# Kernel tuning notes

Hardware: AMD Instinct MI355X
Metric: run time of the kernel (lower is better)

Reference implementation:

```python
import jax, jax.numpy as jnp
import numpy as np

RD = 3  # rec_depth


def _conv_block(x, w, b):
    # x: [B, T, C] -> Conv1d(same padding for odd kernel) + ReLU.
    # AdaptiveMaxPool1d(T) on a length-T input is the identity, so it is omitted.
    pad = (w.shape[-1] - 1) // 2
    xc = jnp.transpose(x, (0, 2, 1))  # [B, C, T]
    out = jax.lax.conv_general_dilated(xc, w, (1,), [(pad, pad)],
                                       dimension_numbers=('NCH', 'OIH', 'NCH'))
    out = jax.nn.relu(out + b[None, :, None])
    return jnp.transpose(out, (0, 2, 1))  # [B, T, n_filters]


def _rhn_cell(x_in, s, WH, WT, RHw, RHb, RTw, RTb):
    # Coupled-gate RHN cell: RD micro-steps of gated highway updates.
    preds = []
    for l in range(RD):
        if l == 0:
            h = jnp.tanh(x_in @ WH + s @ RHw[l] + RHb[l])
            t = jax.nn.sigmoid(x_in @ WT + s @ RTw[l] + RTb[l])
        else:
            h = jnp.tanh(s @ RHw[l] + RHb[l])
            t = jax.nn.sigmoid(s @ RTw[l] + RTb[l])
        s = h * t + (1.0 - t) * s
        preds.append(s)
    return s, preds


def _forward(x, y, conv0_w, conv0_b, conv1_w, conv1_b, c2e_w, c2e_b,
             enc_WH, enc_WT, enc_RHw, enc_RHb, enc_RTw, enc_RTb,
             dec_WH, dec_WT, dec_RHw, dec_RHb, dec_RTw, dec_RTb,
             Tk_w, Uk_w, Uk_b, vk_w, vk_b,
             Wt_w, Vt_w, Vt_b, W_w, W_b, V_w, V_b):
    x = _conv_block(x, conv0_w, conv0_b)
    x = _conv_block(x, conv1_w, conv1_b)
    x = x @ c2e_w + c2e_b                          # [B, T, enc_input_size]
    B, T, _ = x.shape
    NE = enc_WH.shape[1]
    ND = dec_WH.shape[1]

    # ---- RHN encoder: scan over time, emit state after every rec-depth step ----
    def enc_step(s, x_t):
        s, preds = _rhn_cell(x_t, s, enc_WH, enc_WT, enc_RHw, enc_RHb, enc_RTw, enc_RTb)
        return s, jnp.stack(preds, axis=-1)        # [B, NE, RD]

    _, hw = jax.lax.scan(enc_step, jnp.zeros((B, NE), x.dtype), jnp.transpose(x, (1, 0, 2)))
    h = jnp.transpose(hw, (1, 0, 2, 3))            # [B, T, NE, RD] == h_T_L

    # Encoder-side attention projections are decoder-time-invariant: precompute.
    Uh = jnp.einsum('btnr,rnm->rbtm', h, Uk_w) + Uk_b[:, None, None, :]  # [RD, B, T, NE]

    # ---- attentive RHN decoder ----
    def dec_step(carry, y_t):
        s, _ = carry
        Ts = jnp.einsum('bd,rdm->rbm', s, Tk_w)    # T_k(s) broadcast over T
        e = jnp.einsum('rbtm,rm->rbt', jnp.tanh(Uh + Ts[:, :, None, :]), vk_w) \
            + vk_b[:, None, None]                  # [RD, B, T]
        alpha = jax.nn.softmax(e, axis=-1)         # softmax over T
        d = jnp.einsum('rbt,btnr->rbn', alpha, h)  # [RD, B, NE]
        d = jnp.transpose(d, (1, 0, 2)).reshape(B, -1)  # [B, RD*NE], k-major blocks
        y_til = y_t @ Wt_w + d @ Vt_w + Vt_b
        s, _ = _rhn_cell(y_til, s, dec_WH, dec_WT, dec_RHw, dec_RHb, dec_RTw, dec_RTb)
        return (s, d), None

    init = (jnp.zeros((B, ND), x.dtype), jnp.zeros((B, RD * NE), x.dtype))
    (s, d), _ = jax.lax.scan(dec_step, init, jnp.transpose(y, (1, 0, 2)))
    return s @ W_w + W_b + d @ V_w + V_b           # [B, target_feats]


def setup_inputs() -> dict:
    ks = jax.random.split(jax.random.key(0), 24)
    B, T, F, TF = 256, 256, 16, 1
    NF, EI, NE, ND, FS = 64, 64, 128, 128, 5

    def rn(i, shape, s=0.1):
        return jax.random.normal(ks[i], shape, jnp.float32) * s

    z = lambda *shape: jnp.zeros(shape, jnp.float32)
    return {
        'x': jax.random.normal(ks[0], (B, T, F), jnp.float32),
        'y': jax.random.normal(ks[1], (B, T, TF), jnp.float32),
        'conv0_w': rn(2, (NF, F, FS)), 'conv0_b': z(NF),
        'conv1_w': rn(3, (NF, NF, FS)), 'conv1_b': z(NF),
        'c2e_w': rn(4, (NF, EI)), 'c2e_b': z(EI),
        'enc_WH': rn(5, (EI, NE)), 'enc_WT': rn(6, (EI, NE)),
        'enc_RHw': rn(7, (RD, NE, NE)), 'enc_RHb': z(RD, NE),
        'enc_RTw': rn(8, (RD, NE, NE)), 'enc_RTb': z(RD, NE),
        'dec_WH': rn(9, (TF, ND)), 'dec_WT': rn(10, (TF, ND)),
        'dec_RHw': rn(11, (RD, ND, ND)), 'dec_RHb': z(RD, ND),
        'dec_RTw': rn(12, (RD, ND, ND)), 'dec_RTb': z(RD, ND),
        'Tk_w': rn(13, (RD, ND, NE)),
        'Uk_w': rn(14, (RD, NE, NE)), 'Uk_b': z(RD, NE),
        'vk_w': rn(15, (RD, NE)), 'vk_b': z(RD),
        'Wt_w': rn(16, (TF, TF)),
        'Vt_w': rn(17, (RD * NE, TF)), 'Vt_b': z(TF),
        'W_w': rn(18, (ND, TF)), 'W_b': z(TF),
        'V_w': rn(19, (RD * NE, TF)), 'V_b': z(TF),
    }


def reference(x, y, conv0_w, conv0_b, conv1_w, conv1_b, c2e_w, c2e_b,
              enc_WH, enc_WT, enc_RHw, enc_RHb, enc_RTw, enc_RTb,
              dec_WH, dec_WT, dec_RHw, dec_RHb, dec_RTw, dec_RTb,
              Tk_w, Uk_w, Uk_b, vk_w, vk_b,
              Wt_w, Vt_w, Vt_b, W_w, W_b, V_w, V_b):
    return _forward(x, y, conv0_w, conv0_b, conv1_w, conv1_b, c2e_w, c2e_b,
                    enc_WH, enc_WT, enc_RHw, enc_RHb, enc_RTw, enc_RTb,
                    dec_WH, dec_WT, dec_RHw, dec_RHb, dec_RTw, dec_RTb,
                    Tk_w, Uk_w, Uk_b, vk_w, vk_b,
                    Wt_w, Vt_w, Vt_b, W_w, W_b, V_w, V_b)
```

## Files before the change

kernel.cpp:

```cpp
#include <hip/hip_runtime.h>
#include <cstdint>

#define DEV __device__ __forceinline__

typedef unsigned short ushort8 __attribute__((ext_vector_type(8)));
typedef unsigned int uint32;

#if __has_builtin(__builtin_amdgcn_rcpf)
DEV float rcp_fast(float x) { return __builtin_amdgcn_rcpf(x); }
#else
DEV float rcp_fast(float x) { return 1.f / x; }
#endif
#if __has_builtin(__builtin_amdgcn_exp2f)
DEV float exp2_fast(float x) { return __builtin_amdgcn_exp2f(x); }
#else
DEV float exp2_fast(float x) { return exp2f(x); }
#endif

DEV float tanh_fast(float x) {
  float z = exp2_fast(x * 2.8853900817779268f);
  return 1.f - 2.f * rcp_fast(z + 1.f);
}
DEV float sigmoid_fast(float x) {
  return rcp_fast(1.f + exp2_fast(-1.4426950408889634f * x));
}

DEV unsigned short f2bf(float f) {
  uint32 u = __float_as_uint(f);
  u += 0x7FFFu + ((u >> 16) & 1u);
  return (unsigned short)(u >> 16);
}
DEV float bf2f(unsigned short s) { return __uint_as_float(((uint32)s) << 16); }
DEV float bf2f_lo(uint32 u) { return __uint_as_float(u << 16); }
DEV float bf2f_hi(uint32 u) { return __uint_as_float(u & 0xFFFF0000u); }

__global__ __launch_bounds__(256) void k_prep(const float* __restrict__ RHw,
                                              const float* __restrict__ RTw,
                                              uint32* __restrict__ out) {
  int i = blockIdx.x * 256 + threadIdx.x;
  if (i >= 49152) return;
  int g = i / 24576, rem = i % 24576;
  int l = rem / 8192, n2 = (rem >> 7) & 63, m = rem & 127;
  const float* W = g ? RTw : RHw;
  float w0 = W[(size_t)(l * 128 + 2 * n2) * 128 + m];
  float w1 = W[(size_t)(l * 128 + 2 * n2 + 1) * 128 + m];
  out[i] = (uint32)f2bf(w0) | ((uint32)f2bf(w1) << 16);
}

__global__ __launch_bounds__(256) void k_conv0(
    const float* __restrict__ x, const float* __restrict__ w,
    const float* __restrict__ bias, float* __restrict__ out) {
  __shared__ float wl[16 * 5 * 64];
  __shared__ float xl[68 * 16];
  const int blk = blockIdx.x;
  const int b = blk >> 2, tt = blk & 3;
  const int tid = threadIdx.x;
  for (int i = tid; i < 5120; i += 256) {
    int o = i / 80, rem = i % 80, ii = rem / 5, kk = rem % 5;
    wl[(ii * 5 + kk) * 64 + o] = w[i];
  }
  const int t0 = tt * 64;
  for (int i = tid; i < 68 * 16; i += 256) {
    int row = i >> 4, c = i & 15;
    int t = t0 - 2 + row;
    xl[i] = (t >= 0 && t < 256) ? x[((b << 8) + t) * 16 + c] : 0.f;
  }
  __syncthreads();
  const int o = tid & 63, tr = tid >> 6;
  for (int j = 0; j < 16; ++j) {
    int tl = tr * 16 + j;
    float acc = bias[o];
#pragma unroll
    for (int kk = 0; kk < 5; ++kk)
#pragma unroll
      for (int ii = 0; ii < 16; ++ii)
        acc += xl[(tl + kk) * 16 + ii] * wl[(ii * 5 + kk) * 64 + o];
    out[((b << 8) + t0 + tl) * 64 + o] = fmaxf(acc, 0.f);
  }
}

__global__ __launch_bounds__(256) void k_conv1(
    const float* __restrict__ in0, const float* __restrict__ w,
    const float* __restrict__ bias, float* __restrict__ out) {
  __shared__ float wl[64 * 5 * 64];
  __shared__ float xl[68 * 64];
  const int blk = blockIdx.x;
  const int b = blk >> 2, tt = blk & 3;
  const int tid = threadIdx.x;
  for (int i = tid; i < 64 * 5 * 64; i += 256) {
    int o = i / 320, rem = i % 320, ii = rem / 5, kk = rem % 5;
    wl[(ii * 5 + kk) * 64 + o] = w[i];
  }
  const int t0 = tt * 64;
  for (int i = tid; i < 68 * 64; i += 256) {
    int row = i >> 6, c = i & 63;
    int t = t0 - 2 + row;
    xl[i] = (t >= 0 && t < 256) ? in0[((b << 8) + t) * 64 + c] : 0.f;
  }
  __syncthreads();
  const int o = tid & 63, tr = tid >> 6;
  for (int j = 0; j < 16; ++j) {
    int tl = tr * 16 + j;
    float acc = bias[o];
    for (int kk = 0; kk < 5; ++kk) {
#pragma unroll 16
      for (int ii = 0; ii < 64; ++ii)
        acc += xl[(tl + kk) * 64 + ii] * wl[(ii * 5 + kk) * 64 + o];
    }
    out[((b << 8) + t0 + tl) * 64 + o] = fmaxf(acc, 0.f);
  }
}

__global__ __launch_bounds__(256) void k_c2e_proj(
    const float* __restrict__ in1, const float* __restrict__ cw,
    const float* __restrict__ cb, const float* __restrict__ WH,
    const float* __restrict__ WT, float* __restrict__ xph,
    float* __restrict__ xpt) {
  __shared__ float xin[64 * 64];
  __shared__ float w1[64 * 64];
  __shared__ float xe[64 * 64];
  __shared__ float wh[64 * 128];
  __shared__ float wt[64 * 128];
  const int blk = blockIdx.x;
  const int b = blk >> 2, tt = blk & 3;
  const int tid = threadIdx.x;
  for (int i = tid; i < 4096; i += 256) {
    xin[i] = in1[(size_t)(((b << 8) + tt * 64)) * 64 + i];
    w1[i] = cw[i];
  }
  for (int i = tid; i < 8192; i += 256) {
    wh[i] = WH[i];
    wt[i] = WT[i];
  }
  __syncthreads();
  {
    const int o = tid & 63, tr = tid >> 6;
    for (int j = 0; j < 16; ++j) {
      int tl = tr * 16 + j;
      float acc = cb[o];
#pragma unroll 16
      for (int k = 0; k < 64; ++k) acc += xin[tl * 64 + k] * w1[k * 64 + o];
      xe[tl * 64 + o] = acc;
    }
  }
  __syncthreads();
  {
    const int m = tid & 127, hf = tid >> 7;
    for (int j = 0; j < 32; ++j) {
      int tl = hf * 32 + j;
      float a0 = 0.f, a1 = 0.f;
#pragma unroll 16
      for (int k = 0; k < 64; ++k) {
        float xv = xe[tl * 64 + k];
        a0 += xv * wh[k * 128 + m];
        a1 += xv * wt[k * 128 + m];
      }
      size_t oidx = (size_t)((b << 8) + tt * 64 + tl) * 128 + m;
      xph[oidx] = a0;
      xpt[oidx] = a1;
    }
  }
}

__global__ __launch_bounds__(512, 2) void k_encoder(
    const float* __restrict__ xph, const float* __restrict__ xpt,
    const float* __restrict__ RHw, const float* __restrict__ RHb,
    const float* __restrict__ RTw, const float* __restrict__ RTb,
    unsigned short* __restrict__ h_bf) {
  const int b = blockIdx.x;
  const int tid = threadIdx.x;
  const int g = tid >> 8;
  const int m = (tid >> 1) & 127;
  const int hf = tid & 1;
  const float* W = g ? RTw : RHw;
  const float* Bb = g ? RTb : RHb;
  const float* XP = g ? xpt : xph;
  float wreg[3][64];
#pragma unroll
  for (int l = 0; l < 3; ++l)
#pragma unroll
    for (int j = 0; j < 64; ++j)
      wreg[l][j] = W[(size_t)(l * 128 + hf * 64 + j) * 128 + m];
  float bias[3];
#pragma unroll
  for (int l = 0; l < 3; ++l) bias[l] = Bb[l * 128 + m];

  __shared__ float s_lds[128];
  __shared__ float hg[128];
  __shared__ float tg[128];
  if (tid < 128) s_lds[tid] = 0.f;
  __syncthreads();

  for (int t = 0; t < 256; ++t) {
    const float xp = XP[(size_t)((b << 8) + t) * 128 + m];
#pragma unroll
    for (int l = 0; l < 3; ++l) {
      float acc = (hf == 0) ? (bias[l] + (l == 0 ? xp : 0.f)) : 0.f;
      const float* sp = s_lds + hf * 64;
#pragma unroll
      for (int j = 0; j < 64; ++j) acc += sp[j] * wreg[l][j];
      float tot = acc + __shfl_xor(acc, 1);
      if (hf == 0) {
        if (g == 0) hg[m] = tanh_fast(tot);
        else        tg[m] = sigmoid_fast(tot);
      }
      __syncthreads();
      if (tid < 128) {
        float tv = tg[tid];
        float sn = hg[tid] * tv + (1.f - tv) * s_lds[tid];
        s_lds[tid] = sn;
        h_bf[((size_t)(b * 3 + t) * 0 + ((size_t)(b * 3 + l) * 256 + t)) * 128 + tid] = f2bf(sn);
      }
      __syncthreads();
    }
  }
}

__global__ __launch_bounds__(256) void k_uh(
    const unsigned short* __restrict__ h_bf, const float* __restrict__ Uk_w,
    const float* __restrict__ Uk_b, unsigned short* __restrict__ Uh_bf) {
  __shared__ float wl[128 * 128];
  __shared__ float hl[32 * 128];
  const int blk = blockIdx.x;
  const int b = blk / 24;
  const int rem = blk % 24;
  const int r = rem >> 3, tt = rem & 7;
  const int tid = threadIdx.x;
  for (int i = tid; i < 16384; i += 256) wl[i] = Uk_w[(size_t)r * 16384 + i];
  const size_t hbase = ((size_t)(b * 3 + r) * 256 + tt * 32) * 128;
  const ushort8* hv = (const ushort8*)(h_bf + hbase);
  for (int i = tid; i < 512; i += 256) {
    ushort8 u = hv[i];
#pragma unroll
    for (int j = 0; j < 8; ++j) hl[i * 8 + j] = bf2f(u[j]);
  }
  __syncthreads();
  const int m = tid & 127, tr = tid >> 7;
  const float ub = Uk_b[r * 128 + m];
  for (int j = 0; j < 16; ++j) {
    int tl = tr * 16 + j;
    float acc = ub;
#pragma unroll 16
    for (int n = 0; n < 128; ++n) acc += hl[tl * 128 + n] * wl[n * 128 + m];
    Uh_bf[hbase + (size_t)tl * 128 + m] = f2bf(acc);
  }
}

__global__ __launch_bounds__(768) void k_hv(
    const unsigned short* __restrict__ h_bf, const float* __restrict__ Vt_w,
    const float* __restrict__ V_w, float* __restrict__ hv,
    float* __restrict__ hv2) {
  __shared__ float vt[384], vw[384];
  const int b = blockIdx.x, tid = threadIdx.x;
  if (tid < 384) {
    vt[tid] = Vt_w[tid];
    vw[tid] = V_w[tid];
  }
  __syncthreads();
  const int r = tid >> 8;
  const uint2* hp = (const uint2*)(h_bf + ((size_t)b * 768 + tid) * 128);
  const float* vtp = vt + r * 128;
  const float* vwp = vw + r * 128;
  float a1 = 0.f, a2 = 0.f;
#pragma unroll 8
  for (int q = 0; q < 32; ++q) {
    uint2 u = hp[q];
    int m = q * 4;
    float h0 = bf2f_lo(u.x), h1 = bf2f_hi(u.x);
    float h2 = bf2f_lo(u.y), h3 = bf2f_hi(u.y);
    a1 += vtp[m] * h0 + vtp[m + 1] * h1 + vtp[m + 2] * h2 + vtp[m + 3] * h3;
    a2 += vwp[m] * h0 + vwp[m + 1] * h1 + vwp[m + 2] * h2 + vwp[m + 3] * h3;
  }
  hv[(size_t)b * 768 + tid] = a1;
  hv2[(size_t)b * 768 + tid] = a2;
}

__global__ __launch_bounds__(1024, 4) void k_decoder(
    const float* __restrict__ y, const unsigned short* __restrict__ Uh_bf,
    const float* __restrict__ hv_g, const float* __restrict__ hv2_g,
    const float* __restrict__ Tk_w, const float* __restrict__ vk_w,
    const float* __restrict__ vk_b, const float* __restrict__ Wt_w,
    const float* __restrict__ Vt_b, const float* __restrict__ WHd,
    const float* __restrict__ WTd, const uint32* __restrict__ cellw,
    const float* __restrict__ RHb, const float* __restrict__ RTb,
    const float* __restrict__ W_w, const float* __restrict__ W_b,
    const float* __restrict__ V_b, float* __restrict__ out) {
  const int b = blockIdx.x, tid = threadIdx.x;

  __shared__ uint32 tk_lds[24576];
  __shared__ __align__(8) float Ts_lds[3 * 136];
  __shared__ __align__(8) float vk_pad[3 * 136];
  __shared__ __align__(8) float a_lds[768];
  __shared__ __align__(8) float hv_lds[768];
  __shared__ __align__(8) float hv2_lds[768];
  __shared__ __align__(8) float s_lds[128];
  __shared__ float cpart[8 * 128];
  __shared__ float bias_lds[1024];
  __shared__ float y_lds[256];
  __shared__ float redN[12], redD[12], redN2[12];
  __shared__ float ytil_lds;

  for (int i = tid; i < 24576; i += 1024) {
    int r = i >> 13, rem = i & 8191, j = rem >> 7, m = rem & 127;
    float g0 = Tk_w[(size_t)r * 16384 + (2 * j) * 128 + m];
    float g1 = Tk_w[(size_t)r * 16384 + (2 * j + 1) * 128 + m];
    tk_lds[r * 8192 + m * 64 + (j ^ (m & 31))] =
        (uint32)f2bf(g0) | ((uint32)f2bf(g1) << 16);
  }
  if (tid < 384) {
    int r = tid >> 7, m = tid & 127;
    vk_pad[r * 136 + (m >> 5) * 34 + (m & 31)] = vk_w[tid];
    bias_lds[tid] = RHb[tid];
    bias_lds[384 + tid] = RTb[tid];
  }
  if (tid < 128) {
    bias_lds[768 + tid] = WHd[tid];
    bias_lds[896 + tid] = WTd[tid];
    s_lds[tid] = 0.f;
  }
  if (tid < 256) y_lds[tid] = y[(b << 8) + tid];
  if (tid < 768) {
    hv_lds[tid] = hv_g[(size_t)b * 768 + tid];
    hv2_lds[tid] = hv2_g[(size_t)b * 768 + tid];
  }
  const float wt0 = Wt_w[0], vtb0 = Vt_b[0];
  float vkb[3] = {vk_b[0], vk_b[1], vk_b[2]};

  const int t_e4 = tid >> 2, q4 = tid & 3;
  uint32 ureg[3][16];
#pragma unroll
  for (int r = 0; r < 3; ++r) {
    const uint4* up = (const uint4*)(Uh_bf +
        ((size_t)(b * 3 + r) * 256 + t_e4) * 128 + q4 * 32);
#pragma unroll
    for (int q = 0; q < 4; ++q) {
      uint4 v = up[q];
      ureg[r][4 * q + 0] = v.x;
      ureg[r][4 * q + 1] = v.y;
      ureg[r][4 * q + 2] = v.z;
      ureg[r][4 * q + 3] = v.w;
    }
  }
  uint32 zr;
  asm volatile("s_mov_b32 %0, 0" : "=s"(zr));
#pragma unroll
  for (int r = 0; r < 3; ++r)
#pragma unroll
    for (int q = 0; q < 16; ++q) ureg[r][q] ^= zr;
  __syncthreads();

  const int lane = tid & 63, wv = tid >> 6;
  const int r3t = (tid >> 8) & 3, m2 = (tid >> 1) & 127, p2 = tid & 1;
  const int gc = tid >> 9, ch = (tid >> 7) & 3, mc = tid & 127;
  const uint32* Wc = cellw + gc * 24576 + mc;
  const int n2base = ch * 16;

  for (int step = 0; step < 256; ++step) {
    if (tid < 768) {
      const uint32* tkp = tk_lds + r3t * 8192 + m2 * 64;
      const int swz = m2 & 31;
      const float* sp = s_lds + p2 * 64;
      const int jb = p2 * 32;
      float acc = 0.f;
#pragma unroll 8
      for (int jj = 0; jj < 32; ++jj) {
        uint32 w = tkp[(jb + jj) ^ swz];
        float2 sv = *(const float2*)(sp + 2 * jj);
        acc += sv.x * bf2f_lo(w) + sv.y * bf2f_hi(w);
      }
      float tot = acc + __shfl_xor(acc, 1);
      if (p2 == 0) Ts_lds[r3t * 136 + (m2 >> 5) * 34 + (m2 & 31)] = tot;
    }
    __syncthreads();
    {
      float er[3];
#pragma unroll
      for (int r = 0; r < 3; ++r) {
        const float2* ts2 = (const float2*)(Ts_lds + r * 136 + q4 * 34);
        const float2* vk2 = (const float2*)(vk_pad + r * 136 + q4 * 34);
        float acc = 0.f;
#pragma unroll
        for (int j = 0; j < 16; ++j) {
          uint32 w = ureg[r][j];
          float2 t2 = ts2[j], v2 = vk2[j];
          acc += v2.x * tanh_fast(bf2f_lo(w) + t2.x);
          acc += v2.y * tanh_fast(bf2f_hi(w) + t2.y);
        }
        acc += __shfl_xor(acc, 1);
        acc += __shfl_xor(acc, 2);
        er[r] = acc;
      }
      if (q4 == 0) {
#pragma unroll
        for (int r = 0; r < 3; ++r) a_lds[r * 256 + t_e4] = er[r] + vkb[r];
      }
    }
    __syncthreads();
    {
      float pn = 0.f, pd = 0.f, pn2 = 0.f;
      if (tid < 768) {
        float p = __expf(a_lds[tid]);
        pd = p;
        pn = p * hv_lds[tid];
        if (step == 255) pn2 = p * hv2_lds[tid];
      }
#pragma unroll
      for (int off = 32; off; off >>= 1) {
        pn += __shfl_xor(pn, off);
        pd += __shfl_xor(pd, off);
      }
      if (step == 255) {
#pragma unroll
        for (int off = 32; off; off >>= 1) pn2 += __shfl_xor(pn2, off);
      }
      if (lane == 0 && wv < 12) {
        redN[wv] = pn;
        redD[wv] = pd;
        if (step == 255) redN2[wv] = pn2;
      }
    }
    __syncthreads();
    const float2* sp2 = (const float2*)s_lds;
#pragma unroll
    for (int l = 0; l < 3; ++l) {
      {
        float acc = 0.f;
        const uint32* wp = Wc + (size_t)(l * 64 + n2base) * 128;
#pragma unroll 8
        for (int n2 = 0; n2 < 16; ++n2) {
          uint32 w = wp[(size_t)n2 * 128];
          float2 sv = sp2[n2base + n2];
          acc += sv.x * bf2f_lo(w) + sv.y * bf2f_hi(w);
        }
        cpart[(gc * 4 + ch) * 128 + mc] = acc;
        if (l == 0 && tid == 0) {
          float yt = y_lds[step] * wt0 + vtb0;
#pragma unroll
          for (int r = 0; r < 3; ++r) {
            float ns = redN[4 * r] + redN[4 * r + 1] + redN[4 * r + 2] + redN[4 * r + 3];
            float ds = redD[4 * r] + redD[4 * r + 1] + redD[4 * r + 2] + redD[4 * r + 3];
            yt += ns * rcp_fast(ds);
          }
          ytil_lds = yt;
        }
      }
      __syncthreads();
      if (tid < 128) {
        float ha = cpart[tid] + cpart[128 + tid] + cpart[256 + tid] +
                   cpart[384 + tid] + bias_lds[l * 128 + tid];
        float ta = cpart[512 + tid] + cpart[640 + tid] + cpart[768 + tid] +
                   cpart[896 + tid] + bias_lds[384 + l * 128 + tid];
        if (l == 0) {
          float yt = ytil_lds;
          ha += yt * bias_lds[768 + tid];
          ta += yt * bias_lds[896 + tid];
        }
        float hvv = tanh_fast(ha);
        float tv = sigmoid_fast(ta);
        s_lds[tid] = hvv * tv + (1.f - tv) * s_lds[tid];
      }
      __syncthreads();
    }
  }
  if (tid < 64) {
    float acc = s_lds[tid] * W_w[tid] + s_lds[tid + 64] * W_w[tid + 64];
#pragma unroll
    for (int off = 32; off; off >>= 1) acc += __shfl_xor(acc, off);
    if (tid == 0) {
      float o = acc + W_b[0] + V_b[0];
#pragma unroll
      for (int r = 0; r < 3; ++r) {
        float ns = redN2[4 * r] + redN2[4 * r + 1] + redN2[4 * r + 2] + redN2[4 * r + 3];
        float ds = redD[4 * r] + redD[4 * r + 1] + redD[4 * r + 2] + redD[4 * r + 3];
        o += ns * rcp_fast(ds);
      }
      out[b] = o;
    }
  }
}

extern "C" void kernel_launch(void* const* d_in, const int* in_sizes, int n_in,
                              void* d_out, int out_size, void* d_ws,
                              size_t ws_size, hipStream_t stream) {
  (void)in_sizes; (void)n_in; (void)out_size; (void)ws_size;
  const float* x    = (const float*)d_in[0];
  const float* y    = (const float*)d_in[1];
  const float* c0w  = (const float*)d_in[2];
  const float* c0b  = (const float*)d_in[3];
  const float* c1w  = (const float*)d_in[4];
  const float* c1b  = (const float*)d_in[5];
  const float* c2ew = (const float*)d_in[6];
  const float* c2eb = (const float*)d_in[7];
  const float* eWH  = (const float*)d_in[8];
  const float* eWT  = (const float*)d_in[9];
  const float* eRHw = (const float*)d_in[10];
  const float* eRHb = (const float*)d_in[11];
  const float* eRTw = (const float*)d_in[12];
  const float* eRTb = (const float*)d_in[13];
  const float* dWH  = (const float*)d_in[14];
  const float* dWT  = (const float*)d_in[15];
  const float* dRHw = (const float*)d_in[16];
  const float* dRHb = (const float*)d_in[17];
  const float* dRTw = (const float*)d_in[18];
  const float* dRTb = (const float*)d_in[19];
  const float* Tk   = (const float*)d_in[20];
  const float* Ukw  = (const float*)d_in[21];
  const float* Ukb  = (const float*)d_in[22];
  const float* vkw  = (const float*)d_in[23];
  const float* vkb  = (const float*)d_in[24];
  const float* Wtw  = (const float*)d_in[25];
  const float* Vtw  = (const float*)d_in[26];
  const float* Vtb  = (const float*)d_in[27];
  const float* Ww   = (const float*)d_in[28];
  const float* Wb   = (const float*)d_in[29];
  const float* Vw   = (const float*)d_in[30];
  const float* Vb   = (const float*)d_in[31];
  float* out = (float*)d_out;
  float* ws = (float*)d_ws;

  unsigned short* h_bf  = (unsigned short*)ws;
  unsigned short* Uh_bf = (unsigned short*)(ws + 12582912);
  float* xph = ws + 12582912;
  float* xpt = ws + 20971520;
  float* c0o = ws + 29360128;
  float* hv  = ws + 29360128;
  float* hv2 = ws + 30146560;
  float* c1o = ws + 33554432;
  uint32* cellw = (uint32*)(ws + 37748736);

  k_prep<<<192, 256, 0, stream>>>(dRHw, dRTw, cellw);
  k_conv0<<<1024, 256, 0, stream>>>(x, c0w, c0b, c0o);
  k_conv1<<<1024, 256, 0, stream>>>(c0o, c1w, c1b, c1o);
  k_c2e_proj<<<1024, 256, 0, stream>>>(c1o, c2ew, c2eb, eWH, eWT, xph, xpt);
  k_encoder<<<256, 512, 0, stream>>>(xph, xpt, eRHw, eRHb, eRTw, eRTb, h_bf);
  k_uh<<<6144, 256, 0, stream>>>(h_bf, Ukw, Ukb, Uh_bf);
  k_hv<<<256, 768, 0, stream>>>(h_bf, Vtw, Vw, hv, hv2);
  k_decoder<<<256, 1024, 0, stream>>>(y, Uh_bf, hv, hv2, Tk, vkw, vkb, Wtw,
                                      Vtb, dWH, dWT, cellw, dRHb, dRTb,
                                      Ww, Wb, Vb, out);
}
```

Baseline: 5.354 ms.

## Restructure decoder attention and cell matvec with prescaled tanh and double-buffered state

Uh and Tk are prescaled by 2*log2(e), and the attention sum is rewritten as sum(vk) - 2*sum(vk/(1+exp2(.))), so tanh costs one exp2 and one rcp per element. Each thread now holds a whole Uh row (64 registers) instead of quarter rows, which removes the cross-lane score reduction and one barrier per step. The recurrent cell matvec keeps its bf16 weights in registers, prefetching the next layer during the current one. Partial sums are reduced with shuffles instead of a cpart LDS pass, and the state is double-buffered in padded LDS, so each micro-step needs one barrier instead of two. k_uh is also changed to reuse the staged weight across eight time tiles per block, which adds register pressure and changes the rounding of the bf16-scaled values.

```diff
diff --git a/kernel.cpp b/kernel.cpp
--- a/kernel.cpp
+++ b/kernel.cpp
@@ -17,8 +17,10 @@
 DEV float exp2_fast(float x) { return exp2f(x); }
 #endif
 
+#define SCALE2LOG2E 2.8853900817779268f
+
 DEV float tanh_fast(float x) {
-  float z = exp2_fast(x * 2.8853900817779268f);
+  float z = exp2_fast(x * SCALE2LOG2E);
   return 1.f - 2.f * rcp_fast(z + 1.f);
 }
 DEV float sigmoid_fast(float x) {
@@ -33,6 +35,10 @@
 DEV float bf2f(unsigned short s) { return __uint_as_float(((uint32)s) << 16); }
 DEV float bf2f_lo(uint32 u) { return __uint_as_float(u << 16); }
 DEV float bf2f_hi(uint32 u) { return __uint_as_float(u & 0xFFFF0000u); }
+
+DEV int spad_idx(int m) {
+  return (m >> 5) * 34 + ((m >> 1) & 15) * 2 + (m & 1);
+}
 
 __global__ __launch_bounds__(256) void k_prep(const float* __restrict__ RHw,
                                               const float* __restrict__ RTw,
@@ -40,7 +46,8 @@
   int i = blockIdx.x * 256 + threadIdx.x;
   if (i >= 49152) return;
   int g = i / 24576, rem = i % 24576;
-  int l = rem / 8192, n2 = (rem >> 7) & 63, m = rem & 127;
+  int l = rem / 8192, rem2 = rem & 8191;
+  int m = rem2 >> 6, n2 = rem2 & 63;
   const float* W = g ? RTw : RHw;
   float w0 = W[(size_t)(l * 128 + 2 * n2) * 128 + m];
   float w1 = W[(size_t)(l * 128 + 2 * n2 + 1) * 128 + m];
@@ -209,40 +216,41 @@
         float tv = tg[tid];
         float sn = hg[tid] * tv + (1.f - tv) * s_lds[tid];
         s_lds[tid] = sn;
-        h_bf[((size_t)(b * 3 + t) * 0 + ((size_t)(b * 3 + l) * 256 + t)) * 128 + tid] = f2bf(sn);
+        h_bf[((size_t)(b * 3 + l) * 256 + t) * 128 + tid] = f2bf(sn);
       }
       __syncthreads();
     }
   }
 }
 
-__global__ __launch_bounds__(256) void k_uh(
+__global__ __launch_bounds__(256, 2) void k_uh(
     const unsigned short* __restrict__ h_bf, const float* __restrict__ Uk_w,
     const float* __restrict__ Uk_b, unsigned short* __restrict__ Uh_bf) {
   __shared__ float wl[128 * 128];
   __shared__ float hl[32 * 128];
   const int blk = blockIdx.x;
-  const int b = blk / 24;
-  const int rem = blk % 24;
-  const int r = rem >> 3, tt = rem & 7;
+  const int b = blk / 3, r = blk % 3;
   const int tid = threadIdx.x;
   for (int i = tid; i < 16384; i += 256) wl[i] = Uk_w[(size_t)r * 16384 + i];
-  const size_t hbase = ((size_t)(b * 3 + r) * 256 + tt * 32) * 128;
-  const ushort8* hv = (const ushort8*)(h_bf + hbase);
-  for (int i = tid; i < 512; i += 256) {
-    ushort8 u = hv[i];
-#pragma unroll
-    for (int j = 0; j < 8; ++j) hl[i * 8 + j] = bf2f(u[j]);
-  }
-  __syncthreads();
   const int m = tid & 127, tr = tid >> 7;
   const float ub = Uk_b[r * 128 + m];
-  for (int j = 0; j < 16; ++j) {
-    int tl = tr * 16 + j;
-    float acc = ub;
+  for (int tt = 0; tt < 8; ++tt) {
+    const size_t hbase = ((size_t)(b * 3 + r) * 256 + tt * 32) * 128;
+    __syncthreads();
+    const ushort8* hv = (const ushort8*)(h_bf + hbase);
+    for (int i = tid; i < 512; i += 256) {
+      ushort8 u = hv[i];
+#pragma unroll
+      for (int j = 0; j < 8; ++j) hl[i * 8 + j] = bf2f(u[j]);
+    }
+    __syncthreads();
+    for (int j = 0; j < 16; ++j) {
+      int tl = tr * 16 + j;
+      float acc = ub;
 #pragma unroll 16
-    for (int n = 0; n < 128; ++n) acc += hl[tl * 128 + n] * wl[n * 128 + m];
-    Uh_bf[hbase + (size_t)tl * 128 + m] = f2bf(acc);
+      for (int n = 0; n < 128; ++n) acc += hl[tl * 128 + n] * wl[n * 128 + m];
+      Uh_bf[hbase + (size_t)tl * 128 + m] = f2bf(acc * SCALE2LOG2E);
+    }
   }
 }
 
@@ -288,190 +296,187 @@
   const int b = blockIdx.x, tid = threadIdx.x;
 
   __shared__ uint32 tk_lds[24576];
-  __shared__ __align__(8) float Ts_lds[3 * 136];
-  __shared__ __align__(8) float vk_pad[3 * 136];
-  __shared__ __align__(8) float a_lds[768];
-  __shared__ __align__(8) float hv_lds[768];
-  __shared__ __align__(8) float hv2_lds[768];
-  __shared__ __align__(8) float s_lds[128];
-  __shared__ float cpart[8 * 128];
+  __shared__ __align__(16) float tsvk[768];
+  __shared__ float s_pad[2][136];
+  __shared__ float hv_lds[768], hv2_lds[768];
   __shared__ float bias_lds[1024];
   __shared__ float y_lds[256];
   __shared__ float redN[12], redD[12], redN2[12];
-  __shared__ float ytil_lds;
+  __shared__ float svk_lds[3];
 
   for (int i = tid; i < 24576; i += 1024) {
     int r = i >> 13, rem = i & 8191, j = rem >> 7, m = rem & 127;
-    float g0 = Tk_w[(size_t)r * 16384 + (2 * j) * 128 + m];
-    float g1 = Tk_w[(size_t)r * 16384 + (2 * j + 1) * 128 + m];
-    tk_lds[r * 8192 + m * 64 + (j ^ (m & 31))] =
-        (uint32)f2bf(g0) | ((uint32)f2bf(g1) << 16);
+    float g0 = Tk_w[(size_t)r * 16384 + (2 * j) * 128 + m] * SCALE2LOG2E;
+    float g1 = Tk_w[(size_t)r * 16384 + (2 * j + 1) * 128 + m] * SCALE2LOG2E;
+    tk_lds[i] = (uint32)f2bf(g0) | ((uint32)f2bf(g1) << 16);
+  }
+  if (tid < 192) {
+    int r = tid >> 6, j = tid & 63;
+    tsvk[(r * 64 + j) * 4 + 2] = -2.f * vk_w[r * 128 + 2 * j];
+    tsvk[(r * 64 + j) * 4 + 3] = -2.f * vk_w[r * 128 + 2 * j + 1];
+  }
+  if (tid < 3) {
+    float sv = vk_b[tid];
+    for (int m = 0; m < 128; ++m) sv += vk_w[tid * 128 + m];
+    svk_lds[tid] = sv;
   }
   if (tid < 384) {
-    int r = tid >> 7, m = tid & 127;
-    vk_pad[r * 136 + (m >> 5) * 34 + (m & 31)] = vk_w[tid];
     bias_lds[tid] = RHb[tid];
     bias_lds[384 + tid] = RTb[tid];
   }
   if (tid < 128) {
     bias_lds[768 + tid] = WHd[tid];
     bias_lds[896 + tid] = WTd[tid];
-    s_lds[tid] = 0.f;
-  }
+  }
+  if (tid < 272) ((float*)s_pad)[tid] = 0.f;
   if (tid < 256) y_lds[tid] = y[(b << 8) + tid];
   if (tid < 768) {
     hv_lds[tid] = hv_g[(size_t)b * 768 + tid];
     hv2_lds[tid] = hv2_g[(size_t)b * 768 + tid];
   }
   const float wt0 = Wt_w[0], vtb0 = Vt_b[0];
-  float vkb[3] = {vk_b[0], vk_b[1], vk_b[2]};
-
-  const int t_e4 = tid >> 2, q4 = tid & 3;
-  uint32 ureg[3][16];
-#pragma unroll
-  for (int r = 0; r < 3; ++r) {
-    const uint4* up = (const uint4*)(Uh_bf +
-        ((size_t)(b * 3 + r) * 256 + t_e4) * 128 + q4 * 32);
-#pragma unroll
-    for (int q = 0; q < 4; ++q) {
+
+  const int rA = tid >> 8;
+  uint32 ureg[64];
+  {
+    const size_t row = (size_t)b * 768 + (tid < 768 ? tid : (tid & 255));
+    const uint4* up = (const uint4*)(Uh_bf + row * 128);
+#pragma unroll
+    for (int q = 0; q < 16; ++q) {
       uint4 v = up[q];
-      ureg[r][4 * q + 0] = v.x;
-      ureg[r][4 * q + 1] = v.y;
-      ureg[r][4 * q + 2] = v.z;
-      ureg[r][4 * q + 3] = v.w;
+      ureg[4 * q + 0] = v.x;
+      ureg[4 * q + 1] = v.y;
+      ureg[4 * q + 2] = v.z;
+      ureg[4 * q + 3] = v.w;
     }
   }
   uint32 zr;
   asm volatile("s_mov_b32 %0, 0" : "=s"(zr));
 #pragma unroll
-  for (int r = 0; r < 3; ++r)
-#pragma unroll
-    for (int q = 0; q < 16; ++q) ureg[r][q] ^= zr;
+  for (int q = 0; q < 64; ++q) ureg[q] ^= zr;
+
+  const int mC = tid >> 3, sub = tid & 7, gC = sub >> 2, chC = sub & 3;
+  const uint32* wb0 = cellw + ((size_t)(gC * 3) << 13) + (mC << 6) + (chC << 4);
+  uint4 buf0, buf1, buf2, buf3;
+  {
+    const uint4* p = (const uint4*)wb0;
+    buf0 = p[0]; buf1 = p[1]; buf2 = p[2]; buf3 = p[3];
+  }
   __syncthreads();
 
   const int lane = tid & 63, wv = tid >> 6;
-  const int r3t = (tid >> 8) & 3, m2 = (tid >> 1) & 127, p2 = tid & 1;
-  const int gc = tid >> 9, ch = (tid >> 7) & 3, mc = tid & 127;
-  const uint32* Wc = cellw + gc * 24576 + mc;
-  const int n2base = ch * 16;
+  const int m2 = (tid >> 1) & 127, p2 = tid & 1;
+  const int sidx = spad_idx(mC);
+  int spb = 0;
 
   for (int step = 0; step < 256; ++step) {
     if (tid < 768) {
-      const uint32* tkp = tk_lds + r3t * 8192 + m2 * 64;
-      const int swz = m2 & 31;
-      const float* sp = s_lds + p2 * 64;
-      const int jb = p2 * 32;
+      const uint32* tkp = tk_lds + rA * 8192 + m2;
+      const float* sc = s_pad[spb];
       float acc = 0.f;
 #pragma unroll 8
       for (int jj = 0; jj < 32; ++jj) {
-        uint32 w = tkp[(jb + jj) ^ swz];
-        float2 sv = *(const float2*)(sp + 2 * jj);
+        int pr = p2 * 32 + jj;
+        uint32 w = tkp[pr * 128];
+        float2 sv = *(const float2*)(sc + ((pr >> 4) * 17 + (pr & 15)) * 2);
         acc += sv.x * bf2f_lo(w) + sv.y * bf2f_hi(w);
       }
       float tot = acc + __shfl_xor(acc, 1);
-      if (p2 == 0) Ts_lds[r3t * 136 + (m2 >> 5) * 34 + (m2 & 31)] = tot;
+      if (p2 == 0) tsvk[(rA * 64 + (m2 >> 1)) * 4 + (m2 & 1)] = tot;
     }
     __syncthreads();
-    {
-      float er[3];
-#pragma unroll
-      for (int r = 0; r < 3; ++r) {
-        const float2* ts2 = (const float2*)(Ts_lds + r * 136 + q4 * 34);
-        const float2* vk2 = (const float2*)(vk_pad + r * 136 + q4 * 34);
-        float acc = 0.f;
-#pragma unroll
-        for (int j = 0; j < 16; ++j) {
-          uint32 w = ureg[r][j];
-          float2 t2 = ts2[j], v2 = vk2[j];
-          acc += v2.x * tanh_fast(bf2f_lo(w) + t2.x);
-          acc += v2.y * tanh_fast(bf2f_hi(w) + t2.y);
-        }
-        acc += __shfl_xor(acc, 1);
-        acc += __shfl_xor(acc, 2);
-        er[r] = acc;
-      }
-      if (q4 == 0) {
-#pragma unroll
-        for (int r = 0; r < 3; ++r) a_lds[r * 256 + t_e4] = er[r] + vkb[r];
-      }
-    }
-    __syncthreads();
-    {
-      float pn = 0.f, pd = 0.f, pn2 = 0.f;
-      if (tid < 768) {
-        float p = __expf(a_lds[tid]);
-        pd = p;
-        pn = p * hv_lds[tid];
-        if (step == 255) pn2 = p * hv2_lds[tid];
-      }
+    if (tid < 768) {
+      const float4* tv4 = ((const float4*)tsvk) + rA * 64;
+      float acc0 = 0.f, acc1 = 0.f;
+#pragma unroll
+      for (int j = 0; j < 64; ++j) {
+        uint32 w = ureg[j];
+        float4 q = tv4[j];
+        float z0 = exp2_fast(bf2f_lo(w) + q.x);
+        float z1 = exp2_fast(bf2f_hi(w) + q.y);
+        acc0 += q.z * rcp_fast(z0 + 1.f);
+        acc1 += q.w * rcp_fast(z1 + 1.f);
+      }
+      float e = svk_lds[rA] + acc0 + acc1;
+      float p = exp2_fast(e * 1.4426950408889634f);
+      float pn = p * hv_lds[tid];
+      float pd = p;
 #pragma unroll
       for (int off = 32; off; off >>= 1) {
         pn += __shfl_xor(pn, off);
         pd += __shfl_xor(pd, off);
       }
       if (step == 255) {
+        float pn2 = p * hv2_lds[tid];
 #pragma unroll
         for (int off = 32; off; off >>= 1) pn2 += __shfl_xor(pn2, off);
-      }
-      if (lane == 0 && wv < 12) {
+        if (lane == 0) redN2[wv] = pn2;
+      }
+      if (lane == 0) {
         redN[wv] = pn;
         redD[wv] = pd;
-        if (step == 255) redN2[wv] = pn2;
       }
     }
     __syncthreads();
-    const float2* sp2 = (const float2*)s_lds;
+    float ytil = y_lds[step] * wt0 + vtb0;
+#pragma unroll
+    for (int r = 0; r < 3; ++r) {
+      float ns = redN[r * 4] + redN[r * 4 + 1] + redN[r * 4 + 2] + redN[r * 4 + 3];
+      float ds = redD[r * 4] + redD[r * 4 + 1] + redD[r * 4 + 2] + redD[r * 4 + 3];
+      ytil += ns * rcp_fast(ds);
+    }
 #pragma unroll
     for (int l = 0; l < 3; ++l) {
+      const float* sc = s_pad[spb];
+      const float2* sp2 = (const float2*)sc + chC * 17;
+      float acc = 0.f;
+#pragma unroll
+      for (int j = 0; j < 4; ++j) {
+        uint4 w4 = (j == 0) ? buf0 : (j == 1) ? buf1 : (j == 2) ? buf2 : buf3;
+        float2 sa = sp2[j * 4 + 0];
+        acc += sa.x * bf2f_lo(w4.x) + sa.y * bf2f_hi(w4.x);
+        float2 sb = sp2[j * 4 + 1];
+        acc += sb.x * bf2f_lo(w4.y) + sb.y * bf2f_hi(w4.y);
+        float2 sd = sp2[j * 4 + 2];
+        acc += sd.x * bf2f_lo(w4.z) + sd.y * bf2f_hi(w4.z);
+        float2 se = sp2[j * 4 + 3];
+        acc += se.x * bf2f_lo(w4.w) + se.y * bf2f_hi(w4.w);
+      }
       {
-        float acc = 0.f;
-        const uint32* wp = Wc + (size_t)(l * 64 + n2base) * 128;
-#pragma unroll 8
-        for (int n2 = 0; n2 < 16; ++n2) {
-          uint32 w = wp[(size_t)n2 * 128];
-          float2 sv = sp2[n2base + n2];
-          acc += sv.x * bf2f_lo(w) + sv.y * bf2f_hi(w);
-        }
-        cpart[(gc * 4 + ch) * 128 + mc] = acc;
-        if (l == 0 && tid == 0) {
-          float yt = y_lds[step] * wt0 + vtb0;
-#pragma unroll
-          for (int r = 0; r < 3; ++r) {
-            float ns = redN[4 * r] + redN[4 * r + 1] + redN[4 * r + 2] + redN[4 * r + 3];
-            float ds = redD[4 * r] + redD[4 * r + 1] + redD[4 * r + 2] + redD[4 * r + 3];
-            yt += ns * rcp_fast(ds);
-          }
-          ytil_lds = yt;
-        }
-      }
+        const int ln = (l == 2) ? 0 : (l + 1);
+        const uint4* p = (const uint4*)(wb0 + (ln << 13));
+        buf0 = p[0]; buf1 = p[1]; buf2 = p[2]; buf3 = p[3];
+      }
+      acc += __shfl_xor(acc, 1);
+      acc += __shfl_xor(acc, 2);
+      float other = __shfl_xor(acc, 4);
+      float hsum = gC ? other : acc;
+      float tsum = gC ? acc : other;
+      float s_old = sc[sidx];
+      float ha = hsum + bias_lds[l * 128 + mC];
+      float ta = tsum + bias_lds[384 + l * 128 + mC];
+      if (l == 0) {
+        ha += ytil * bias_lds[768 + mC];
+        ta += ytil * bias_lds[896 + mC];
+      }
+      float hvv = tanh_fast(ha);
+      float tv = sigmoid_fast(ta);
+      if (sub == 0) s_pad[spb ^ 1][sidx] = hvv * tv + (1.f - tv) * s_old;
       __syncthreads();
-      if (tid < 128) {
-        float ha = cpart[tid] + cpart[128 + tid] + cpart[256 + tid] +
-                   cpart[384 + tid] + bias_lds[l * 128 + tid];
-        float ta = cpart[512 + tid] + cpart[640 + tid] + cpart[768 + tid] +
-                   cpart[896 + tid] + bias_lds[384 + l * 128 + tid];
-        if (l == 0) {
-          float yt = ytil_lds;
-          ha += yt * bias_lds[768 + tid];
-          ta += yt * bias_lds[896 + tid];
-        }
-        float hvv = tanh_fast(ha);
-        float tv = sigmoid_fast(ta);
-        s_lds[tid] = hvv * tv + (1.f - tv) * s_lds[tid];
-      }
-      __syncthreads();
+      spb ^= 1;
     }
   }
   if (tid < 64) {
-    float acc = s_lds[tid] * W_w[tid] + s_lds[tid + 64] * W_w[tid + 64];
+    const float* sc = s_pad[spb];
+    float acc = sc[spad_idx(tid)] * W_w[tid] + sc[spad_idx(tid + 64)] * W_w[tid + 64];
 #pragma unroll
     for (int off = 32; off; off >>= 1) acc += __shfl_xor(acc, off);
     if (tid == 0) {
       float o = acc + W_b[0] + V_b[0];
 #pragma unroll
       for (int r = 0; r < 3; ++r) {
-        float ns = redN2[4 * r] + redN2[4 * r + 1] + redN2[4 * r + 2] + redN2[4 * r + 3];
-        float ds = redD[4 * r] + redD[4 * r + 1] + redD[4 * r + 2] + redD[4 * r + 3];
+        float ns = redN2[r * 4] + redN2[r * 4 + 1] + redN2[r * 4 + 2] + redN2[r * 4 + 3];
+        float ds = redD[r * 4] + redD[r * 4 + 1] + redD[r * 4 + 2] + redD[r * 4 + 3];
         o += ns * rcp_fast(ds);
       }
       out[b] = o;
@@ -533,7 +538,7 @@
   k_conv1<<<1024, 256, 0, stream>>>(c0o, c1w, c1b, c1o);
   k_c2e_proj<<<1024, 256, 0, stream>>>(c1o, c2ew, c2eb, eWH, eWT, xph, xpt);
   k_encoder<<<256, 512, 0, stream>>>(xph, xpt, eRHw, eRHb, eRTw, eRTb, h_bf);
-  k_uh<<<6144, 256, 0, stream>>>(h_bf, Ukw, Ukb, Uh_bf);
+  k_uh<<<768, 256, 0, stream>>>(h_bf, Ukw, Ukb, Uh_bf);
   k_hv<<<256, 768, 0, stream>>>(h_bf, Vtw, Vw, hv, hv2);
   k_decoder<<<256, 1024, 0, stream>>>(y, Uh_bf, hv, hv2, Tk, vkw, vkb, Wtw,
                                       Vtb, dWH, dWT, cellw, dRHb, dRTb,
```

After: 8.255 ms. 1.54x slower.

## Fold tanh scaling into attention weights and reuse Uk_w tile across time in k_uh

Applied to the files above, without the earlier changes.

Uh and Tk are pre-scaled by 2*log2(e), and vk is scaled by -2 with its sum folded into a per-rank bias. The decoder's attention tanh then becomes a bare exp2 plus reciprocal, with the partial sums split across two accumulators. k_uh now processes all 8 time tiles per (batch, rank) block, so the 64KB Uk_w tile is loaded into LDS once instead of eight times, at the cost of 8x fewer blocks. The rescaled bf16 storage of Uh and Tk slightly changes rounding.

```diff
diff --git a/kernel.cpp b/kernel.cpp
--- a/kernel.cpp
+++ b/kernel.cpp
@@ -17,12 +17,15 @@
 DEV float exp2_fast(float x) { return exp2f(x); }
 #endif
 
+#define SCALE2LOG2E 2.8853900817779268f
+#define LOG2E 1.4426950408889634f
+
 DEV float tanh_fast(float x) {
-  float z = exp2_fast(x * 2.8853900817779268f);
+  float z = exp2_fast(x * SCALE2LOG2E);
   return 1.f - 2.f * rcp_fast(z + 1.f);
 }
 DEV float sigmoid_fast(float x) {
-  return rcp_fast(1.f + exp2_fast(-1.4426950408889634f * x));
+  return rcp_fast(1.f + exp2_fast(-LOG2E * x));
 }
 
 DEV unsigned short f2bf(float f) {
@@ -209,40 +212,41 @@
         float tv = tg[tid];
         float sn = hg[tid] * tv + (1.f - tv) * s_lds[tid];
         s_lds[tid] = sn;
-        h_bf[((size_t)(b * 3 + t) * 0 + ((size_t)(b * 3 + l) * 256 + t)) * 128 + tid] = f2bf(sn);
+        h_bf[((size_t)(b * 3 + l) * 256 + t) * 128 + tid] = f2bf(sn);
       }
       __syncthreads();
     }
   }
 }
 
-__global__ __launch_bounds__(256) void k_uh(
+__global__ __launch_bounds__(256, 2) void k_uh(
     const unsigned short* __restrict__ h_bf, const float* __restrict__ Uk_w,
     const float* __restrict__ Uk_b, unsigned short* __restrict__ Uh_bf) {
   __shared__ float wl[128 * 128];
   __shared__ float hl[32 * 128];
   const int blk = blockIdx.x;
-  const int b = blk / 24;
-  const int rem = blk % 24;
-  const int r = rem >> 3, tt = rem & 7;
+  const int b = blk / 3, r = blk % 3;
   const int tid = threadIdx.x;
   for (int i = tid; i < 16384; i += 256) wl[i] = Uk_w[(size_t)r * 16384 + i];
-  const size_t hbase = ((size_t)(b * 3 + r) * 256 + tt * 32) * 128;
-  const ushort8* hv = (const ushort8*)(h_bf + hbase);
-  for (int i = tid; i < 512; i += 256) {
-    ushort8 u = hv[i];
-#pragma unroll
-    for (int j = 0; j < 8; ++j) hl[i * 8 + j] = bf2f(u[j]);
-  }
-  __syncthreads();
   const int m = tid & 127, tr = tid >> 7;
   const float ub = Uk_b[r * 128 + m];
-  for (int j = 0; j < 16; ++j) {
-    int tl = tr * 16 + j;
-    float acc = ub;
+  for (int tt = 0; tt < 8; ++tt) {
+    const size_t hbase = ((size_t)(b * 3 + r) * 256 + tt * 32) * 128;
+    __syncthreads();
+    const ushort8* hv = (const ushort8*)(h_bf + hbase);
+    for (int i = tid; i < 512; i += 256) {
+      ushort8 u = hv[i];
+#pragma unroll
+      for (int j = 0; j < 8; ++j) hl[i * 8 + j] = bf2f(u[j]);
+    }
+    __syncthreads();
+    for (int j = 0; j < 16; ++j) {
+      int tl = tr * 16 + j;
+      float acc = ub;
 #pragma unroll 16
-    for (int n = 0; n < 128; ++n) acc += hl[tl * 128 + n] * wl[n * 128 + m];
-    Uh_bf[hbase + (size_t)tl * 128 + m] = f2bf(acc);
+      for (int n = 0; n < 128; ++n) acc += hl[tl * 128 + n] * wl[n * 128 + m];
+      Uh_bf[hbase + (size_t)tl * 128 + m] = f2bf(acc * SCALE2LOG2E);
+    }
   }
 }
 
@@ -291,27 +295,32 @@
   __shared__ __align__(8) float Ts_lds[3 * 136];
   __shared__ __align__(8) float vk_pad[3 * 136];
   __shared__ __align__(8) float a_lds[768];
-  __shared__ __align__(8) float hv_lds[768];
-  __shared__ __align__(8) float hv2_lds[768];
+  __shared__ float hv_lds[768], hv2_lds[768];
   __shared__ __align__(8) float s_lds[128];
   __shared__ float cpart[8 * 128];
   __shared__ float bias_lds[1024];
   __shared__ float y_lds[256];
   __shared__ float redN[12], redD[12], redN2[12];
+  __shared__ float svk_lds[3];
   __shared__ float ytil_lds;
 
   for (int i = tid; i < 24576; i += 1024) {
     int r = i >> 13, rem = i & 8191, j = rem >> 7, m = rem & 127;
-    float g0 = Tk_w[(size_t)r * 16384 + (2 * j) * 128 + m];
-    float g1 = Tk_w[(size_t)r * 16384 + (2 * j + 1) * 128 + m];
+    float g0 = Tk_w[(size_t)r * 16384 + (2 * j) * 128 + m] * SCALE2LOG2E;
+    float g1 = Tk_w[(size_t)r * 16384 + (2 * j + 1) * 128 + m] * SCALE2LOG2E;
     tk_lds[r * 8192 + m * 64 + (j ^ (m & 31))] =
         (uint32)f2bf(g0) | ((uint32)f2bf(g1) << 16);
   }
   if (tid < 384) {
     int r = tid >> 7, m = tid & 127;
-    vk_pad[r * 136 + (m >> 5) * 34 + (m & 31)] = vk_w[tid];
+    vk_pad[r * 136 + (m >> 5) * 34 + (m & 31)] = -2.f * vk_w[tid];
     bias_lds[tid] = RHb[tid];
     bias_lds[384 + tid] = RTb[tid];
+  }
+  if (tid < 3) {
+    float sv = vk_b[tid];
+    for (int m = 0; m < 128; ++m) sv += vk_w[tid * 128 + m];
+    svk_lds[tid] = sv;
   }
   if (tid < 128) {
     bias_lds[768 + tid] = WHd[tid];
@@ -324,7 +333,6 @@
     hv2_lds[tid] = hv2_g[(size_t)b * 768 + tid];
   }
   const float wt0 = Wt_w[0], vtb0 = Vt_b[0];
-  float vkb[3] = {vk_b[0], vk_b[1], vk_b[2]};
 
   const int t_e4 = tid >> 2, q4 = tid & 3;
   uint32 ureg[3][16];
@@ -378,21 +386,24 @@
       for (int r = 0; r < 3; ++r) {
         const float2* ts2 = (const float2*)(Ts_lds + r * 136 + q4 * 34);
         const float2* vk2 = (const float2*)(vk_pad + r * 136 + q4 * 34);
-        float acc = 0.f;
+        float acc0 = 0.f, acc1 = 0.f;
 #pragma unroll
         for (int j = 0; j < 16; ++j) {
           uint32 w = ureg[r][j];
           float2 t2 = ts2[j], v2 = vk2[j];
-          acc += v2.x * tanh_fast(bf2f_lo(w) + t2.x);
-          acc += v2.y * tanh_fast(bf2f_hi(w) + t2.y);
+          float z0 = exp2_fast(bf2f_lo(w) + t2.x);
+          float z1 = exp2_fast(bf2f_hi(w) + t2.y);
+          acc0 += v2.x * rcp_fast(z0 + 1.f);
+          acc1 += v2.y * rcp_fast(z1 + 1.f);
         }
-        acc += __shfl_xor(acc, 1);
-        acc += __shfl_xor(acc, 2);
-        er[r] = acc;
+        float a = acc0 + acc1;
+        a += __shfl_xor(a, 1);
+        a += __shfl_xor(a, 2);
+        er[r] = a;
       }
       if (q4 == 0) {
 #pragma unroll
-        for (int r = 0; r < 3; ++r) a_lds[r * 256 + t_e4] = er[r] + vkb[r];
+        for (int r = 0; r < 3; ++r) a_lds[r * 256 + t_e4] = er[r] + svk_lds[r];
       }
     }
     __syncthreads();
@@ -412,11 +423,11 @@
       if (step == 255) {
 #pragma unroll
         for (int off = 32; off; off >>= 1) pn2 += __shfl_xor(pn2, off);
+        if (lane == 0 && wv < 12) redN2[wv] = pn2;
       }
       if (lane == 0 && wv < 12) {
         redN[wv] = pn;
         redD[wv] = pd;
-        if (step == 255) redN2[wv] = pn2;
       }
     }
     __syncthreads();
@@ -533,7 +544,7 @@
   k_conv1<<<1024, 256, 0, stream>>>(c0o, c1w, c1b, c1o);
   k_c2e_proj<<<1024, 256, 0, stream>>>(c1o, c2ew, c2eb, eWH, eWT, xph, xpt);
   k_encoder<<<256, 512, 0, stream>>>(xph, xpt, eRHw, eRHb, eRTw, eRTb, h_bf);
-  k_uh<<<6144, 256, 0, stream>>>(h_bf, Ukw, Ukb, Uh_bf);
+  k_uh<<<768, 256, 0, stream>>>(h_bf, Ukw, Ukb, Uh_bf);
   k_hv<<<256, 768, 0, stream>>>(h_bf, Vtw, Vw, hv, hv2);
   k_decoder<<<256, 1024, 0, stream>>>(y, Uh_bf, hv, hv2, Tk, vkw, vkb, Wtw,
                                       Vtb, dWH, dWT, cellw, dRHb, dRTb,
```

Result: faster. 4.901 ms (-8.5%).
